# Performance work log

Hardware: AMD Instinct MI355X
Metric: run time of the kernel (lower is better)

## Reference

```python
import jax, jax.numpy as jnp
import numpy as np

N = 262144
IN_DIM = 1024
HID = 256
E = 16
TOP_K = 2


def setup_inputs() -> dict:
    key = jax.random.key(0)
    k1, k2, k3, k4, k5 = jax.random.split(key, 5)
    x = jax.random.normal(k1, (N, IN_DIM), dtype=jnp.float32)
    # Kaiming-ish init scaled for stability
    W1 = jax.random.normal(k2, (IN_DIM, HID), dtype=jnp.float32) * (1.0 / np.sqrt(IN_DIM))
    b1 = jnp.zeros((HID,), dtype=jnp.float32)
    W2 = jax.random.normal(k3, (HID, E), dtype=jnp.float32) * (1.0 / np.sqrt(HID))
    b2 = jnp.zeros((E,), dtype=jnp.float32)
    return {"x": x, "W1": W1, "b1": b1, "W2": W2, "b2": b2}


def reference(x, W1, b1, W2, b2):
    # MLP router: Linear -> ELU -> Linear
    h = jax.nn.elu(x @ W1 + b1)            # [N, HID]
    logits = h @ W2 + b2                   # [N, E]
    # top-k mask: keep top-k logits, set the rest to -inf (scatter semantics)
    vals, idx = jax.lax.top_k(logits, TOP_K)          # [N, K]
    rows = jnp.arange(logits.shape[0])[:, None]        # [N, 1]
    masked = jnp.full_like(logits, -jnp.inf).at[rows, idx].set(vals)
    alpha = jax.nn.softmax(masked, axis=-1)            # [N, E]
    return alpha, logits
```

## Files before the change

kernel.cpp:

```cpp
#include <hip/hip_runtime.h>
#include <math.h>

#define KDIM 1024
#define HID 256
#define NE 16
#define ROWS_BLK 128
#define KCH 32
#define NCHUNK 32
#define CH_BYTES 32768
#define W2T_PLANE (NE * HID)
#define ABUF(i) ((i) * 16384)
#define BBUF(i) (32768 + (i) * 32768)
#define SMEM_BYTES 163840

typedef __attribute__((ext_vector_type(8))) _Float16 f16x8;
typedef __attribute__((ext_vector_type(16))) float f32x16;
typedef __attribute__((ext_vector_type(4))) float f32x4;

__device__ __forceinline__ void gld16(const void* g, void* s) {
  __builtin_amdgcn_global_load_lds(
      (const __attribute__((address_space(1))) void*)g,
      (__attribute__((address_space(3))) void*)s, 16, 0, 0);
}

__global__ void prep_w1(const float* __restrict__ W1, _Float16* __restrict__ img) {
  int idx = blockIdx.x * 256 + threadIdx.x;
  int col = idx & 255, kgl = idx >> 8;
  int c = kgl >> 2, kg = kgl & 3, k8 = kgl * 8;
  f16x8 p1, p2;
#pragma unroll
  for (int i = 0; i < 8; ++i) {
    float v = W1[(size_t)(k8 + i) * HID + col];
    _Float16 a = (_Float16)v;
    _Float16 b = (_Float16)((v - (float)a) * 4096.0f);
    p1[i] = a; p2[i] = b;
  }
  size_t off = (size_t)c * 16384 + (size_t)kg * 2048 + (size_t)col * 8;
  *(f16x8*)(img + off) = p1;
  *(f16x8*)(img + off + 8192) = p2;
}

__global__ void prep_w2(const float* __restrict__ W2, _Float16* __restrict__ w2t) {
  int idx = blockIdx.x * 256 + threadIdx.x;
  int e = idx & 15, k = idx >> 4;
  float v = W2[(size_t)k * NE + e];
  _Float16 a = (_Float16)v;
  _Float16 b = (_Float16)((v - (float)a) * 4096.0f);
  w2t[(size_t)e * HID + k] = a;
  w2t[W2T_PLANE + (size_t)e * HID + k] = b;
}

__global__ __launch_bounds__(512, 2) void fused_router(
    const float* __restrict__ x, const _Float16* __restrict__ w1img,
    const _Float16* __restrict__ w2t, const float* __restrict__ bias1,
    const float* __restrict__ bias2, float* __restrict__ outA,
    float* __restrict__ outL)
{
  extern __shared__ char smem[];
  const int t = threadIdx.x, l = t & 63, w = t >> 6;
  const int rowg = w >> 2, colg = w & 3;
  const int l31 = l & 31, hi = l >> 5;
  const int R0 = blockIdx.x * ROWS_BLK;
  const int arow0 = rowg * 64 + l31;
  const int bcol0 = colg * 64 + l31;

  const int xr = t >> 2, xq = t & 3;
  const float* xbase = x + (size_t)(R0 + xr) * KDIM + xq * 8;

  const char* ibase = (const char*)w1img + t * 16;

  f32x16 acc0[2][2], accA[2][2];
#pragma unroll
  for (int rt = 0; rt < 2; ++rt)
#pragma unroll
    for (int ct = 0; ct < 2; ++ct)
#pragma unroll
      for (int j = 0; j < 16; ++j) { acc0[rt][ct][j] = 0.f; accA[rt][ct][j] = 0.f; }

  float xvA[8], xvB[8];

#define XLOADV(XV_, C_) do {                                                  \
    *(float4*)(XV_)     = *(const float4*)(xbase + (size_t)(C_) * KCH);       \
    *(float4*)((XV_)+4) = *(const float4*)(xbase + (size_t)(C_) * KCH + 4);   \
  } while (0)

#define BSTAGE_H(C_, BUF_, H_) do {                                           \
    const char* is_ = ibase + (size_t)(C_) * CH_BYTES + (H_) * 16384;         \
    char* bd_ = smem + BBUF(BUF_) + (H_) * 16384 + t * 16;                    \
    gld16(is_,        bd_);                                                   \
    gld16(is_ + 8192, bd_ + 8192);                                            \
  } while (0)

#define ASPLITV(XV_, ABW_) do {                                               \
    f16x8 pa_, pb_;                                                           \
    _Pragma("unroll") for (int j_ = 0; j_ < 8; ++j_) {                        \
      float v_ = (XV_)[j_];                                                   \
      _Float16 a_ = (_Float16)v_;                                             \
      _Float16 b_ = (_Float16)((v_ - (float)a_) * 4096.0f);                   \
      pa_[j_] = a_; pb_[j_] = b_;                                             \
    }                                                                         \
    int ao_ = ABUF(ABW_) + xq * 2048 + xr * 16;                               \
    *(f16x8*)(smem + ao_) = pa_;                                              \
    *(f16x8*)(smem + ao_ + 8192) = pb_;                                       \
  } while (0)

#define PHASE(S_, ABR_, BBR_) do {                                            \
    const int gg_ = 2 * (S_) + hi;                                            \
    f16x8 a1_[2], a2_[2];                                                     \
    _Pragma("unroll") for (int rt_ = 0; rt_ < 2; ++rt_) {                     \
      int ao_ = ABUF(ABR_) + gg_ * 2048 + (arow0 + 32 * rt_) * 16;            \
      a1_[rt_] = *(const f16x8*)(smem + ao_);                                 \
      a2_[rt_] = *(const f16x8*)(smem + ao_ + 8192);                          \
    }                                                                         \
    __builtin_amdgcn_s_setprio(1);                                            \
    _Pragma("unroll") for (int ct_ = 0; ct_ < 2; ++ct_) {                     \
      int bo_ = BBUF(BBR_) + gg_ * 4096 + (bcol0 + 32 * ct_) * 16;            \
      f16x8 b1_ = *(const f16x8*)(smem + bo_);                                \
      f16x8 b2_ = *(const f16x8*)(smem + bo_ + 16384);                        \
      _Pragma("unroll") for (int rt_ = 0; rt_ < 2; ++rt_) {                   \
        acc0[rt_][ct_] = __builtin_amdgcn_mfma_f32_32x32x16_f16(              \
            a1_[rt_], b1_, acc0[rt_][ct_], 0, 0, 0);                          \
        accA[rt_][ct_] = __builtin_amdgcn_mfma_f32_32x32x16_f16(              \
            a1_[rt_], b2_, accA[rt_][ct_], 0, 0, 0);                          \
        accA[rt_][ct_] = __builtin_amdgcn_mfma_f32_32x32x16_f16(              \
            a2_[rt_], b1_, accA[rt_][ct_], 0, 0, 0);                          \
      }                                                                       \
    }                                                                         \
    __builtin_amdgcn_s_setprio(0);                                            \
  } while (0)

#define BODY(C_, ABR_, ABW_, BBR_, BBS_, XV_) do {                            \
    if ((C_) + 2 < NCHUNK) { BSTAGE_H((C_)+2, BBS_, 0); BSTAGE_H((C_)+2, BBS_, 1); } \
    if ((C_) + 1 < NCHUNK) ASPLITV(XV_, ABW_);                                \
    if ((C_) + 3 < NCHUNK) XLOADV(XV_, (C_) + 3);                             \
    PHASE(0, ABR_, BBR_);                                                     \
    PHASE(1, ABR_, BBR_);                                                     \
    __builtin_amdgcn_sched_barrier(0);                                        \
    if ((C_) <= NCHUNK - 4) {                                                 \
      asm volatile("s_waitcnt vmcnt(6)" ::: "memory");                        \
    } else if ((C_) == NCHUNK - 3) {                                          \
      asm volatile("s_waitcnt vmcnt(4)" ::: "memory");                        \
    } else {                                                                  \
      asm volatile("s_waitcnt vmcnt(0)" ::: "memory");                        \
    }                                                                         \
    asm volatile("s_waitcnt lgkmcnt(0)" ::: "memory");                        \
    __builtin_amdgcn_sched_barrier(0);                                        \
    __builtin_amdgcn_s_barrier();                                             \
    __builtin_amdgcn_sched_barrier(0);                                        \
  } while (0)

  XLOADV(xvA, 0);
  XLOADV(xvB, 1);
  BSTAGE_H(0, 0, 0); BSTAGE_H(0, 0, 1);
  BSTAGE_H(1, 1, 0); BSTAGE_H(1, 1, 1);
  ASPLITV(xvA, 0);
  XLOADV(xvA, 2);
  asm volatile("s_waitcnt vmcnt(6)" ::: "memory");
  asm volatile("s_waitcnt lgkmcnt(0)" ::: "memory");
  __builtin_amdgcn_sched_barrier(0);
  __builtin_amdgcn_s_barrier();
  __builtin_amdgcn_sched_barrier(0);

#pragma unroll 1
  for (int cb = 0; cb < NCHUNK; cb += 4) {
    BODY(cb + 0, 0, 1, 0, 2, xvB);
    BODY(cb + 1, 1, 0, 1, 3, xvA);
    BODY(cb + 2, 0, 1, 2, 0, xvB);
    BODY(cb + 3, 1, 0, 3, 1, xvA);
  }

  const float c12 = 1.0f / 4096.0f;
  const int tok = l & 15, g2 = l >> 4;

#pragma unroll 1
  for (int p = 0; p < 2; ++p) {
    __syncthreads();
    if (rowg == p) {
#pragma unroll
      for (int ct = 0; ct < 2; ++ct) {
        int col = bcol0 + 32 * ct;
        float bc = bias1[col];
        int cg = col >> 3, cb = (col & 7) * 2;
#pragma unroll
        for (int rt = 0; rt < 2; ++rt) {
#pragma unroll
          for (int r = 0; r < 16; ++r) {
            int tloc = 32 * rt + (r & 3) + 8 * (r >> 2) + 4 * hi;
            float v = acc0[rt][ct][r] + c12 * accA[rt][ct][r] + bc;
            v = v > 0.f ? v : expm1f(v);
            _Float16 h1 = (_Float16)v;
            _Float16 h2 = (_Float16)((v - (float)h1) * 4096.0f);
            int off = tloc * 512 + ((cg ^ (tloc & 7)) << 4) + cb;
            *(_Float16*)(smem + off) = h1;
            *(_Float16*)(smem + 32768 + off) = h2;
          }
        }
      }
    }
    __syncthreads();
    if (w < 4) {
      int tloc = w * 16 + tok;
      f32x4 L0, LA;
#pragma unroll
      for (int j = 0; j < 4; ++j) { L0[j] = 0.f; LA[j] = 0.f; }
      const _Float16* w2a = w2t + (size_t)tok * HID;
      const _Float16* w2b = w2a + W2T_PLANE;
#pragma unroll
      for (int kt = 0; kt < 8; ++kt) {
        int gg = (kt * 4 + g2) ^ (tloc & 7);
        f16x8 hb1 = *(const f16x8*)(smem + tloc * 512 + (gg << 4));
        f16x8 hb2 = *(const f16x8*)(smem + 32768 + tloc * 512 + (gg << 4));
        f16x8 wa = *(const f16x8*)(w2a + kt * 32 + 8 * g2);
        f16x8 wb = *(const f16x8*)(w2b + kt * 32 + 8 * g2);
        L0 = __builtin_amdgcn_mfma_f32_16x16x32_f16(wa, hb1, L0, 0, 0, 0);
        LA = __builtin_amdgcn_mfma_f32_16x16x32_f16(wa, hb2, LA, 0, 0, 0);
        LA = __builtin_amdgcn_mfma_f32_16x16x32_f16(wb, hb1, LA, 0, 0, 0);
      }
      float4 b2v = *(const float4*)(bias2 + 4 * g2);
      float L[4];
      L[0] = L0[0] + c12 * LA[0] + b2v.x;
      L[1] = L0[1] + c12 * LA[1] + b2v.y;
      L[2] = L0[2] + c12 * LA[2] + b2v.z;
      L[3] = L0[3] + c12 * LA[3] + b2v.w;

      float o1[4], o2[4], o3[4];
#pragma unroll
      for (int j = 0; j < 4; ++j) o1[j] = __shfl_xor(L[j], 16);
#pragma unroll
      for (int j = 0; j < 4; ++j) o2[j] = __shfl_xor(L[j], 32);
#pragma unroll
      for (int j = 0; j < 4; ++j) o3[j] = __shfl_xor(o1[j], 32);

      float all16[16];
#pragma unroll
      for (int cq = 0; cq < 4; ++cq) {
        int xg = cq ^ g2;
#pragma unroll
        for (int j = 0; j < 4; ++j) {
          float v = L[j];
          v = (xg == 1) ? o1[j] : v;
          v = (xg == 2) ? o2[j] : v;
          v = (xg == 3) ? o3[j] : v;
          all16[cq * 4 + j] = v;
        }
      }

      int i1 = 0; float m1 = all16[0];
#pragma unroll
      for (int e = 1; e < 16; ++e) { if (all16[e] > m1) { m1 = all16[e]; i1 = e; } }
      int i2 = -1; float m2 = -INFINITY;
#pragma unroll
      for (int e = 0; e < 16; ++e) { if (e != i1 && all16[e] > m2) { m2 = all16[e]; i2 = e; } }
      float ex = expf(m2 - m1);
      float sden = 1.f + ex;
      float A1 = 1.f / sden;
      float A2 = ex / sden;

      int e0 = 4 * g2;
      float4 alv;
      alv.x = (e0 + 0 == i1) ? A1 : ((e0 + 0 == i2) ? A2 : 0.f);
      alv.y = (e0 + 1 == i1) ? A1 : ((e0 + 1 == i2) ? A2 : 0.f);
      alv.z = (e0 + 2 == i1) ? A1 : ((e0 + 2 == i2) ? A2 : 0.f);
      alv.w = (e0 + 3 == i1) ? A1 : ((e0 + 3 == i2) ? A2 : 0.f);

      size_t orow = (size_t)(R0 + p * 64 + tloc);
      float4 lgv; lgv.x = L[0]; lgv.y = L[1]; lgv.z = L[2]; lgv.w = L[3];
      *(float4*)(outL + orow * NE + e0) = lgv;
      *(float4*)(outA + orow * NE + e0) = alv;
    }
  }
#undef XLOADV
#undef BSTAGE_H
#undef ASPLITV
#undef PHASE
#undef BODY
}

extern "C" void kernel_launch(void* const* d_in, const int* in_sizes, int n_in,
                              void* d_out, int out_size, void* d_ws, size_t ws_size,
                              hipStream_t stream) {
  const float* x  = (const float*)d_in[0];
  const float* W1 = (const float*)d_in[1];
  const float* b1 = (const float*)d_in[2];
  const float* W2 = (const float*)d_in[3];
  const float* b2 = (const float*)d_in[4];
  _Float16* w1img = (_Float16*)d_ws;
  _Float16* w2t = w1img + (size_t)NCHUNK * (CH_BYTES / 2);
  float* outA = (float*)d_out;
  const size_t n_tok = (size_t)in_sizes[0] / KDIM;
  float* outL = outA + n_tok * NE;

  prep_w1<<<dim3(128), dim3(256), 0, stream>>>(W1, w1img);
  prep_w2<<<dim3(16), dim3(256), 0, stream>>>(W2, w2t);

  hipFuncSetAttribute((const void*)fused_router,
                      hipFuncAttributeMaxDynamicSharedMemorySize, SMEM_BYTES);
  fused_router<<<dim3((unsigned)(n_tok / ROWS_BLK)), dim3(512), SMEM_BYTES, stream>>>(
      x, w1img, w2t, b1, b2, outA, outL);
}
```

Measured before the change: 602.8 us.

## Load W1 B-operand fragments directly into registers instead of staging through LDS

Replaces the global_load_lds staging of W1 chunks into a 4-slot shared-memory ring with per-lane direct global loads of the B fragments into register double buffers. LDS shrinks from 160KB to 64KB, and the explicit vmcnt waits and sched barriers are dropped. The aim is to cut LDS traffic and shared-memory capacity pressure. The cost is that every wave redundantly fetches its B fragments from global/L2 and register pressure rises, with prefetch depth reduced from two chunks to one.

```diff
diff --git a/kernel.cpp b/kernel.cpp
--- a/kernel.cpp
+++ b/kernel.cpp
@@ -10,18 +10,11 @@
 #define CH_BYTES 32768
 #define W2T_PLANE (NE * HID)
 #define ABUF(i) ((i) * 16384)
-#define BBUF(i) (32768 + (i) * 32768)
-#define SMEM_BYTES 163840
+#define SMEM_BYTES 65536
 
 typedef __attribute__((ext_vector_type(8))) _Float16 f16x8;
 typedef __attribute__((ext_vector_type(16))) float f32x16;
 typedef __attribute__((ext_vector_type(4))) float f32x4;
-
-__device__ __forceinline__ void gld16(const void* g, void* s) {
-  __builtin_amdgcn_global_load_lds(
-      (const __attribute__((address_space(1))) void*)g,
-      (__attribute__((address_space(3))) void*)s, 16, 0, 0);
-}
 
 __global__ void prep_w1(const float* __restrict__ W1, _Float16* __restrict__ img) {
   int idx = blockIdx.x * 256 + threadIdx.x;
@@ -67,7 +60,7 @@
   const int xr = t >> 2, xq = t & 3;
   const float* xbase = x + (size_t)(R0 + xr) * KDIM + xq * 8;
 
-  const char* ibase = (const char*)w1img + t * 16;
+  const char* bimg = (const char*)w1img + (size_t)bcol0 * 16 + (size_t)hi * 4096;
 
   f32x16 acc0[2][2], accA[2][2];
 #pragma unroll
@@ -78,17 +71,20 @@
       for (int j = 0; j < 16; ++j) { acc0[rt][ct][j] = 0.f; accA[rt][ct][j] = 0.f; }
 
   float xvA[8], xvB[8];
+  f16x8 bsetA[8], bsetB[8];
 
 #define XLOADV(XV_, C_) do {                                                  \
     *(float4*)(XV_)     = *(const float4*)(xbase + (size_t)(C_) * KCH);       \
     *(float4*)((XV_)+4) = *(const float4*)(xbase + (size_t)(C_) * KCH + 4);   \
   } while (0)
 
-#define BSTAGE_H(C_, BUF_, H_) do {                                           \
-    const char* is_ = ibase + (size_t)(C_) * CH_BYTES + (H_) * 16384;         \
-    char* bd_ = smem + BBUF(BUF_) + (H_) * 16384 + t * 16;                    \
-    gld16(is_,        bd_);                                                   \
-    gld16(is_ + 8192, bd_ + 8192);                                            \
+#define BLOADR(BS_, C_) do {                                                  \
+    const char* bp_ = bimg + (size_t)(C_) * CH_BYTES;                         \
+    _Pragma("unroll") for (int i_ = 0; i_ < 8; ++i_) {                        \
+      const int off_ = ((i_ >> 2) & 1) * 8192 + ((i_ >> 1) & 1) * 512         \
+                     + (i_ & 1) * 16384;                                      \
+      BS_[i_] = *(const f16x8*)(bp_ + off_);                                  \
+    }                                                                         \
   } while (0)
 
 #define ASPLITV(XV_, ABW_) do {                                               \
@@ -104,69 +100,52 @@
     *(f16x8*)(smem + ao_ + 8192) = pb_;                                       \
   } while (0)
 
-#define PHASE(S_, ABR_, BBR_) do {                                            \
-    const int gg_ = 2 * (S_) + hi;                                            \
-    f16x8 a1_[2], a2_[2];                                                     \
-    _Pragma("unroll") for (int rt_ = 0; rt_ < 2; ++rt_) {                     \
-      int ao_ = ABUF(ABR_) + gg_ * 2048 + (arow0 + 32 * rt_) * 16;            \
-      a1_[rt_] = *(const f16x8*)(smem + ao_);                                 \
-      a2_[rt_] = *(const f16x8*)(smem + ao_ + 8192);                          \
+#define COMPUTE(AR_, BS_) do {                                                \
+    _Pragma("unroll") for (int s_ = 0; s_ < 2; ++s_) {                        \
+      const int gg_ = 2 * s_ + hi;                                            \
+      f16x8 a1_[2], a2_[2];                                                   \
+      _Pragma("unroll") for (int rt_ = 0; rt_ < 2; ++rt_) {                   \
+        int ao_ = ABUF(AR_) + gg_ * 2048 + (arow0 + 32 * rt_) * 16;           \
+        a1_[rt_] = *(const f16x8*)(smem + ao_);                               \
+        a2_[rt_] = *(const f16x8*)(smem + ao_ + 8192);                        \
+      }                                                                       \
+      __builtin_amdgcn_s_setprio(1);                                          \
+      _Pragma("unroll") for (int ct_ = 0; ct_ < 2; ++ct_)                     \
+      _Pragma("unroll") for (int rt_ = 0; rt_ < 2; ++rt_)                     \
+        acc0[rt_][ct_] = __builtin_amdgcn_mfma_f32_32x32x16_f16(              \
+            a1_[rt_], BS_[4 * s_ + 2 * ct_ + 0], acc0[rt_][ct_], 0, 0, 0);    \
+      _Pragma("unroll") for (int ct_ = 0; ct_ < 2; ++ct_)                     \
+      _Pragma("unroll") for (int rt_ = 0; rt_ < 2; ++rt_)                     \
+        accA[rt_][ct_] = __builtin_amdgcn_mfma_f32_32x32x16_f16(              \
+            a1_[rt_], BS_[4 * s_ + 2 * ct_ + 1], accA[rt_][ct_], 0, 0, 0);    \
+      _Pragma("unroll") for (int ct_ = 0; ct_ < 2; ++ct_)                     \
+      _Pragma("unroll") for (int rt_ = 0; rt_ < 2; ++rt_)                     \
+        accA[rt_][ct_] = __builtin_amdgcn_mfma_f32_32x32x16_f16(              \
+            a2_[rt_], BS_[4 * s_ + 2 * ct_ + 0], accA[rt_][ct_], 0, 0, 0);    \
+      __builtin_amdgcn_s_setprio(0);                                          \
     }                                                                         \
-    __builtin_amdgcn_s_setprio(1);                                            \
-    _Pragma("unroll") for (int ct_ = 0; ct_ < 2; ++ct_) {                     \
-      int bo_ = BBUF(BBR_) + gg_ * 4096 + (bcol0 + 32 * ct_) * 16;            \
-      f16x8 b1_ = *(const f16x8*)(smem + bo_);                                \
-      f16x8 b2_ = *(const f16x8*)(smem + bo_ + 16384);                        \
-      _Pragma("unroll") for (int rt_ = 0; rt_ < 2; ++rt_) {                   \
-        acc0[rt_][ct_] = __builtin_amdgcn_mfma_f32_32x32x16_f16(              \
-            a1_[rt_], b1_, acc0[rt_][ct_], 0, 0, 0);                          \
-        accA[rt_][ct_] = __builtin_amdgcn_mfma_f32_32x32x16_f16(              \
-            a1_[rt_], b2_, accA[rt_][ct_], 0, 0, 0);                          \
-        accA[rt_][ct_] = __builtin_amdgcn_mfma_f32_32x32x16_f16(              \
-            a2_[rt_], b1_, accA[rt_][ct_], 0, 0, 0);                          \
-      }                                                                       \
-    }                                                                         \
-    __builtin_amdgcn_s_setprio(0);                                            \
-  } while (0)
-
-#define BODY(C_, ABR_, ABW_, BBR_, BBS_, XV_) do {                            \
-    if ((C_) + 2 < NCHUNK) { BSTAGE_H((C_)+2, BBS_, 0); BSTAGE_H((C_)+2, BBS_, 1); } \
-    if ((C_) + 1 < NCHUNK) ASPLITV(XV_, ABW_);                                \
-    if ((C_) + 3 < NCHUNK) XLOADV(XV_, (C_) + 3);                             \
-    PHASE(0, ABR_, BBR_);                                                     \
-    PHASE(1, ABR_, BBR_);                                                     \
-    __builtin_amdgcn_sched_barrier(0);                                        \
-    if ((C_) <= NCHUNK - 4) {                                                 \
-      asm volatile("s_waitcnt vmcnt(6)" ::: "memory");                        \
-    } else if ((C_) == NCHUNK - 3) {                                          \
-      asm volatile("s_waitcnt vmcnt(4)" ::: "memory");                        \
-    } else {                                                                  \
-      asm volatile("s_waitcnt vmcnt(0)" ::: "memory");                        \
-    }                                                                         \
+  } while (0)
+
+#define BODY(C_, AR_, AW_, BCUR_, BNXT_, XC_, XL_) do {                       \
+    if ((C_) + 1 < NCHUNK) BLOADR(BNXT_, (C_) + 1);                           \
+    if ((C_) + 2 < NCHUNK) XLOADV(XL_, (C_) + 2);                             \
+    if ((C_) + 1 < NCHUNK) ASPLITV(XC_, AW_);                                 \
+    COMPUTE(AR_, BCUR_);                                                      \
     asm volatile("s_waitcnt lgkmcnt(0)" ::: "memory");                        \
-    __builtin_amdgcn_sched_barrier(0);                                        \
     __builtin_amdgcn_s_barrier();                                             \
-    __builtin_amdgcn_sched_barrier(0);                                        \
   } while (0)
 
   XLOADV(xvA, 0);
+  BLOADR(bsetA, 0);
   XLOADV(xvB, 1);
-  BSTAGE_H(0, 0, 0); BSTAGE_H(0, 0, 1);
-  BSTAGE_H(1, 1, 0); BSTAGE_H(1, 1, 1);
   ASPLITV(xvA, 0);
-  XLOADV(xvA, 2);
-  asm volatile("s_waitcnt vmcnt(6)" ::: "memory");
   asm volatile("s_waitcnt lgkmcnt(0)" ::: "memory");
-  __builtin_amdgcn_sched_barrier(0);
   __builtin_amdgcn_s_barrier();
-  __builtin_amdgcn_sched_barrier(0);
 
 #pragma unroll 1
-  for (int cb = 0; cb < NCHUNK; cb += 4) {
-    BODY(cb + 0, 0, 1, 0, 2, xvB);
-    BODY(cb + 1, 1, 0, 1, 3, xvA);
-    BODY(cb + 2, 0, 1, 2, 0, xvB);
-    BODY(cb + 3, 1, 0, 3, 1, xvA);
+  for (int cb = 0; cb < NCHUNK; cb += 2) {
+    BODY(cb,     0, 1, bsetA, bsetB, xvB, xvA);
+    BODY(cb + 1, 1, 0, bsetB, bsetA, xvA, xvB);
   }
 
   const float c12 = 1.0f / 4096.0f;
@@ -270,9 +249,9 @@
     }
   }
 #undef XLOADV
-#undef BSTAGE_H
+#undef BLOADR
 #undef ASPLITV
-#undef PHASE
+#undef COMPUTE
 #undef BODY
 }
 
```

After: 642.1 us. 6.5% more time.

## Restructure main loop into double-buffered two-phase pipeline with smaller LDS footprint

Applied to the files above, without the earlier changes.

Replaces the 4-deep B-buffer ring and 3-ahead x prefetch with a 2-deep double buffer. Each chunk is split into two phases that read fragments, issue the next chunk's staging, then run the MFMAs between barriers. LDS use drops from 160KB to 96KB, which may let more blocks fit per CU. The cost is shallower prefetch and more barriers per chunk, which can expose global load latency.

```diff
diff --git a/kernel.cpp b/kernel.cpp
--- a/kernel.cpp
+++ b/kernel.cpp
@@ -10,8 +10,9 @@
 #define CH_BYTES 32768
 #define W2T_PLANE (NE * HID)
 #define ABUF(i) ((i) * 16384)
-#define BBUF(i) (32768 + (i) * 32768)
-#define SMEM_BYTES 163840
+#define BBASE 32768
+#define BB_STRIDE 32768
+#define SMEM_BYTES 98304
 
 typedef __attribute__((ext_vector_type(8))) _Float16 f16x8;
 typedef __attribute__((ext_vector_type(16))) float f32x16;
@@ -84,13 +85,6 @@
     *(float4*)((XV_)+4) = *(const float4*)(xbase + (size_t)(C_) * KCH + 4);   \
   } while (0)
 
-#define BSTAGE_H(C_, BUF_, H_) do {                                           \
-    const char* is_ = ibase + (size_t)(C_) * CH_BYTES + (H_) * 16384;         \
-    char* bd_ = smem + BBUF(BUF_) + (H_) * 16384 + t * 16;                    \
-    gld16(is_,        bd_);                                                   \
-    gld16(is_ + 8192, bd_ + 8192);                                            \
-  } while (0)
-
 #define ASPLITV(XV_, ABW_) do {                                               \
     f16x8 pa_, pb_;                                                           \
     _Pragma("unroll") for (int j_ = 0; j_ < 8; ++j_) {                        \
@@ -104,70 +98,94 @@
     *(f16x8*)(smem + ao_ + 8192) = pb_;                                       \
   } while (0)
 
-#define PHASE(S_, ABR_, BBR_) do {                                            \
-    const int gg_ = 2 * (S_) + hi;                                            \
-    f16x8 a1_[2], a2_[2];                                                     \
+#define BSTAGE_H(C1_, BUF_, H_) do {                                          \
+    const char* is_ = ibase + (size_t)(C1_) * CH_BYTES + (H_) * 16384;        \
+    char* bd_ = smem + BBASE + (BUF_) * BB_STRIDE + (H_) * 16384 + t * 16;    \
+    gld16(is_,        bd_);                                                   \
+    gld16(is_ + 8192, bd_ + 8192);                                            \
+  } while (0)
+
+#define FRAG_READ(PI_, S_)                                                    \
+    f16x8 a1_[2], a2_[2], b1_[2], b2_[2];                                     \
+    {                                                                         \
+      const int gg_ = 2 * (S_) + hi;                                          \
+      _Pragma("unroll") for (int rt_ = 0; rt_ < 2; ++rt_) {                   \
+        int ao_ = ABUF(PI_) + gg_ * 2048 + (arow0 + 32 * rt_) * 16;           \
+        a1_[rt_] = *(const f16x8*)(smem + ao_);                               \
+        a2_[rt_] = *(const f16x8*)(smem + ao_ + 8192);                        \
+      }                                                                       \
+      _Pragma("unroll") for (int ct_ = 0; ct_ < 2; ++ct_) {                   \
+        int bo_ = BBASE + (PI_) * BB_STRIDE + gg_ * 4096                      \
+                  + (bcol0 + 32 * ct_) * 16;                                  \
+        b1_[ct_] = *(const f16x8*)(smem + bo_);                               \
+        b2_[ct_] = *(const f16x8*)(smem + bo_ + 16384);                       \
+      }                                                                       \
+    }
+
+#define MFMA12() do {                                                         \
+    __builtin_amdgcn_s_setprio(1);                                            \
+    _Pragma("unroll") for (int ct_ = 0; ct_ < 2; ++ct_)                       \
     _Pragma("unroll") for (int rt_ = 0; rt_ < 2; ++rt_) {                     \
-      int ao_ = ABUF(ABR_) + gg_ * 2048 + (arow0 + 32 * rt_) * 16;            \
-      a1_[rt_] = *(const f16x8*)(smem + ao_);                                 \
-      a2_[rt_] = *(const f16x8*)(smem + ao_ + 8192);                          \
-    }                                                                         \
-    __builtin_amdgcn_s_setprio(1);                                            \
-    _Pragma("unroll") for (int ct_ = 0; ct_ < 2; ++ct_) {                     \
-      int bo_ = BBUF(BBR_) + gg_ * 4096 + (bcol0 + 32 * ct_) * 16;            \
-      f16x8 b1_ = *(const f16x8*)(smem + bo_);                                \
-      f16x8 b2_ = *(const f16x8*)(smem + bo_ + 16384);                        \
-      _Pragma("unroll") for (int rt_ = 0; rt_ < 2; ++rt_) {                   \
-        acc0[rt_][ct_] = __builtin_amdgcn_mfma_f32_32x32x16_f16(              \
-            a1_[rt_], b1_, acc0[rt_][ct_], 0, 0, 0);                          \
-        accA[rt_][ct_] = __builtin_amdgcn_mfma_f32_32x32x16_f16(              \
-            a1_[rt_], b2_, accA[rt_][ct_], 0, 0, 0);                          \
-        accA[rt_][ct_] = __builtin_amdgcn_mfma_f32_32x32x16_f16(              \
-            a2_[rt_], b1_, accA[rt_][ct_], 0, 0, 0);                          \
-      }                                                                       \
+      acc0[rt_][ct_] = __builtin_amdgcn_mfma_f32_32x32x16_f16(                \
+          a1_[rt_], b1_[ct_], acc0[rt_][ct_], 0, 0, 0);                       \
+      accA[rt_][ct_] = __builtin_amdgcn_mfma_f32_32x32x16_f16(                \
+          a1_[rt_], b2_[ct_], accA[rt_][ct_], 0, 0, 0);                       \
+      accA[rt_][ct_] = __builtin_amdgcn_mfma_f32_32x32x16_f16(                \
+          a2_[rt_], b1_[ct_], accA[rt_][ct_], 0, 0, 0);                       \
     }                                                                         \
     __builtin_amdgcn_s_setprio(0);                                            \
   } while (0)
 
-#define BODY(C_, ABR_, ABW_, BBR_, BBS_, XV_) do {                            \
-    if ((C_) + 2 < NCHUNK) { BSTAGE_H((C_)+2, BBS_, 0); BSTAGE_H((C_)+2, BBS_, 1); } \
-    if ((C_) + 1 < NCHUNK) ASPLITV(XV_, ABW_);                                \
-    if ((C_) + 3 < NCHUNK) XLOADV(XV_, (C_) + 3);                             \
-    PHASE(0, ABR_, BBR_);                                                     \
-    PHASE(1, ABR_, BBR_);                                                     \
-    __builtin_amdgcn_sched_barrier(0);                                        \
-    if ((C_) <= NCHUNK - 4) {                                                 \
-      asm volatile("s_waitcnt vmcnt(6)" ::: "memory");                        \
-    } else if ((C_) == NCHUNK - 3) {                                          \
-      asm volatile("s_waitcnt vmcnt(4)" ::: "memory");                        \
-    } else {                                                                  \
-      asm volatile("s_waitcnt vmcnt(0)" ::: "memory");                        \
+#define PH0(C_, PI_, STG_) do {                                               \
+    FRAG_READ(PI_, 0)                                                         \
+    if (STG_) BSTAGE_H((C_) + 1, (PI_) ^ 1, 0);                               \
+    __builtin_amdgcn_s_barrier();                                             \
+    asm volatile("s_waitcnt lgkmcnt(0)" ::: "memory");                        \
+    __builtin_amdgcn_sched_barrier(0);                                        \
+    MFMA12();                                                                 \
+    __builtin_amdgcn_s_barrier();                                             \
+  } while (0)
+
+#define PH1(C_, PI_, STG_, XNXT_, XL_, XLD_, VMSTR_) do {                     \
+    FRAG_READ(PI_, 1)                                                         \
+    if (STG_) {                                                               \
+      BSTAGE_H((C_) + 1, (PI_) ^ 1, 1);                                       \
+      ASPLITV(XNXT_, (PI_) ^ 1);                                              \
     }                                                                         \
+    __builtin_amdgcn_sched_barrier(0);                                        \
+    if (XL_) XLOADV(XLD_, (C_) + 2);                                          \
+    __builtin_amdgcn_sched_barrier(0);                                        \
+    __builtin_amdgcn_s_barrier();                                             \
     asm volatile("s_waitcnt lgkmcnt(0)" ::: "memory");                        \
     __builtin_amdgcn_sched_barrier(0);                                        \
+    MFMA12();                                                                 \
+    __builtin_amdgcn_sched_barrier(0);                                        \
+    asm volatile("s_waitcnt vmcnt(" VMSTR_ ")" ::: "memory");                 \
+    __builtin_amdgcn_sched_barrier(0);                                        \
     __builtin_amdgcn_s_barrier();                                             \
-    __builtin_amdgcn_sched_barrier(0);                                        \
   } while (0)
 
   XLOADV(xvA, 0);
   XLOADV(xvB, 1);
-  BSTAGE_H(0, 0, 0); BSTAGE_H(0, 0, 1);
-  BSTAGE_H(1, 1, 0); BSTAGE_H(1, 1, 1);
+  BSTAGE_H(0, 0, 0);
+  BSTAGE_H(0, 0, 1);
   ASPLITV(xvA, 0);
-  XLOADV(xvA, 2);
-  asm volatile("s_waitcnt vmcnt(6)" ::: "memory");
+  asm volatile("s_waitcnt vmcnt(0)" ::: "memory");
   asm volatile("s_waitcnt lgkmcnt(0)" ::: "memory");
   __builtin_amdgcn_sched_barrier(0);
   __builtin_amdgcn_s_barrier();
-  __builtin_amdgcn_sched_barrier(0);
 
 #pragma unroll 1
-  for (int cb = 0; cb < NCHUNK; cb += 4) {
-    BODY(cb + 0, 0, 1, 0, 2, xvB);
-    BODY(cb + 1, 1, 0, 1, 3, xvA);
-    BODY(cb + 2, 0, 1, 2, 0, xvB);
-    BODY(cb + 3, 1, 0, 3, 1, xvA);
+  for (int cb = 0; cb < NCHUNK - 2; cb += 2) {
+    PH0(cb, 0, 1);
+    PH1(cb, 0, 1, xvB, 1, xvA, "2");
+    PH0(cb + 1, 1, 1);
+    PH1(cb + 1, 1, 1, xvA, 1, xvB, "2");
   }
+  PH0(30, 0, 1);
+  PH1(30, 0, 1, xvB, 0, xvA, "0");
+  PH0(31, 1, 0);
+  PH1(31, 1, 0, xvA, 0, xvB, "0");
 
   const float c12 = 1.0f / 4096.0f;
   const int tok = l & 15, g2 = l >> 4;
@@ -270,10 +288,12 @@
     }
   }
 #undef XLOADV
+#undef ASPLITV
 #undef BSTAGE_H
-#undef ASPLITV
-#undef PHASE
-#undef BODY
+#undef FRAG_READ
+#undef MFMA12
+#undef PH0
+#undef PH1
 }
 
 extern "C" void kernel_launch(void* const* d_in, const int* in_sizes, int n_in,
```

Result: slower. 627.6 us (+4.1%).
